# Kernel optimization log

Measured on AMD Instinct MI355X. Metric: run time of the kernel, lower is better.

The kernel has to match this reference:

```python
import jax, jax.numpy as jnp
import numpy as np

D_MODEL = 1024
N_HEADS = 16
D_K = D_MODEL // N_HEADS
ROPE_THETA = 10000.0


def setup_inputs() -> dict:
    key = jax.random.key(0)
    ks = jax.random.split(key, 5)
    B, S = 2, 2048
    std = (2.0 / (D_MODEL + D_MODEL)) ** 0.5
    x = jax.random.normal(ks[0], (B, S, D_MODEL), dtype=jnp.float32)
    Wq = jax.random.normal(ks[1], (D_MODEL, D_MODEL), dtype=jnp.float32) * std
    Wk = jax.random.normal(ks[2], (D_MODEL, D_MODEL), dtype=jnp.float32) * std
    Wv = jax.random.normal(ks[3], (D_MODEL, D_MODEL), dtype=jnp.float32) * std
    Wo = jax.random.normal(ks[4], (D_MODEL, D_MODEL), dtype=jnp.float32) * std
    token_positions = jnp.arange(S, dtype=jnp.int64 if jax.config.jax_enable_x64 else jnp.int32)
    return {"x": x, "Wq": Wq, "Wk": Wk, "Wv": Wv, "Wo": Wo,
            "token_positions": token_positions}


def _apply_rope(t, token_positions):
    # t: [B, H, S, d_k]; token_positions: [S]
    inv_freq = 1.0 / (ROPE_THETA ** (jnp.arange(0, D_K, 2, dtype=jnp.float32) / D_K))  # [d_k/2]
    freqs = token_positions.astype(jnp.float32)[:, None] * inv_freq[None, :]  # [S, d_k/2]
    cos, sin = jnp.cos(freqs), jnp.sin(freqs)
    x1, x2 = t[..., ::2], t[..., 1::2]
    xr = x1 * cos - x2 * sin
    yr = x1 * sin + x2 * cos
    # interleave back to even/odd positions
    out = jnp.stack([xr, yr], axis=-1).reshape(t.shape)
    return out


def reference(x, Wq, Wk, Wv, Wo, token_positions):
    B, S, D = x.shape
    H, dk = N_HEADS, D_K
    # projections: weight is [d_out, d_in], applied as x @ W.T
    def proj_heads(W):
        y = jnp.einsum('bsd,ed->bse', x, W)
        return y.reshape(B, S, H, dk).transpose(0, 2, 1, 3)  # [B,H,S,dk]
    q = proj_heads(Wq)
    k = proj_heads(Wk)
    v = proj_heads(Wv)
    q = _apply_rope(q, token_positions)
    k = _apply_rope(k, token_positions)
    scores = jnp.einsum('bhqd,bhkd->bhqk', q, k) / jnp.sqrt(jnp.float32(dk))
    causal = jnp.tril(jnp.ones((S, S), dtype=bool))
    scores = jnp.where(causal, scores, -jnp.inf)
    attn = jax.nn.softmax(scores, axis=-1)
    out = jnp.einsum('bhqk,bhkd->bhqd', attn, v)  # [B,H,S,dk]
    out = out.transpose(0, 2, 1, 3).reshape(B, S, D)
    return jnp.einsum('bsd,ed->bse', out, Wo)
```

## Files before the change

kernel.cpp:

```cpp
#include <hip/hip_runtime.h>

typedef __bf16 bf16x8 __attribute__((ext_vector_type(8)));
typedef float f32x4 __attribute__((ext_vector_type(4)));
typedef unsigned short u16x8 __attribute__((ext_vector_type(8)));


__device__ __forceinline__ unsigned short f2bf(float f) {
  unsigned u = __builtin_bit_cast(unsigned, f);
  u = (u + 0x7FFFu + ((u >> 16) & 1u)) >> 16;
  return (unsigned short)u;
}

__device__ __forceinline__ unsigned cvt_pk_bf16(float lo, float hi) {
  unsigned r;
  asm("v_cvt_pk_bf16_f32 %0, %1, %2" : "=v"(r) : "v"(lo), "v"(hi));
  return r;
}

__device__ __forceinline__ void load_lds16(const void* g, void* l) {
  __builtin_amdgcn_global_load_lds(
      (__attribute__((address_space(1))) void*)g,
      (__attribute__((address_space(3))) void*)l, 16, 0, 0);
}

__global__ __launch_bounds__(256) void k_convert(
    const float* __restrict__ x,
    const float* __restrict__ wq, const float* __restrict__ wk,
    const float* __restrict__ wv, const float* __restrict__ wo,
    unsigned short* __restrict__ xb,
    unsigned short* __restrict__ wqb, unsigned short* __restrict__ wkb,
    unsigned short* __restrict__ wvb, unsigned short* __restrict__ wob) {
  const int g = blockIdx.x * 256 + threadIdx.x;
  const float* src;
  unsigned short* dst;
  int off;
  if (g < (1 << 20)) {
    src = x; dst = xb; off = g;
  } else {
    const int q = g - (1 << 20);
    const int t = q >> 18;
    off = q & ((1 << 18) - 1);
    src = (t == 0) ? wq : (t == 1) ? wk : (t == 2) ? wv : wo;
    dst = (t == 0) ? wqb : (t == 1) ? wkb : (t == 2) ? wvb : wob;
  }
  const float4 v = ((const float4*)src)[off];
  ushort4 r;
  r.x = f2bf(v.x); r.y = f2bf(v.y); r.z = f2bf(v.z); r.w = f2bf(v.w);
  ((ushort4*)dst)[off] = r;
}

__global__ __launch_bounds__(256) void k_rope_tab(const int* __restrict__ tpos,
                                                  float* __restrict__ ct,
                                                  float* __restrict__ st) {
  const int idx = blockIdx.x * 256 + threadIdx.x;
  const int s = idx >> 5, i = idx & 31;
  const double p = (double)tpos[s];
  const double f = p * pow(10000.0, -(double)(2 * i) / 64.0);
  ct[idx] = (float)cos(f);
  st[idx] = (float)sin(f);
}

__device__ __forceinline__ void gemm_core_1024(
    const unsigned short* __restrict__ Ag,
    const unsigned short* __restrict__ Bg,
    unsigned short* As, unsigned short* Bs, f32x4 (&acc)[4][4], int tid) {
  const int lane = tid & 63;
  const int w = tid >> 6;
  const int wm = (w >> 1) * 64;
  const int wn = (w & 1) * 64;
  const int lr = lane & 15;
  const int lg8 = (lane >> 4) * 8;
  const int c0 = tid, c1 = 256 + tid;
  const int ar0 = c0 >> 2, ac0 = (c0 & 3) * 8;
  const int ar1 = c1 >> 2, ac1 = (c1 & 3) * 8;

  auto stage = [&](int buf, int kt) {
    unsigned short* Ab = As + buf * 4096;
    unsigned short* Bb = Bs + buf * 4096;
    load_lds16(Ag + ar0 * 1024 + kt + ac0, Ab + c0 * 8);
    load_lds16(Ag + ar1 * 1024 + kt + ac1, Ab + c1 * 8);
    load_lds16(Bg + ar0 * 1024 + kt + ac0, Bb + c0 * 8);
    load_lds16(Bg + ar1 * 1024 + kt + ac1, Bb + c1 * 8);
  };

  stage(0, 0);
  stage(1, 32);
  int cur = 0;
  for (int ki = 0; ki < 32; ++ki) {
    if (ki + 2 < 32) {
      int nb = cur + 2; if (nb >= 3) nb -= 3;
      stage(nb, (ki + 2) * 32);
      asm volatile("s_waitcnt vmcnt(8)" ::: "memory");
    } else if (ki + 1 < 32) {
      asm volatile("s_waitcnt vmcnt(4)" ::: "memory");
    } else {
      asm volatile("s_waitcnt vmcnt(0)" ::: "memory");
    }
    __builtin_amdgcn_s_barrier();
    const unsigned short* Ab = As + cur * 4096;
    const unsigned short* Bb = Bs + cur * 4096;
    bf16x8 af[4], bfv[4];
#pragma unroll
    for (int mi = 0; mi < 4; ++mi)
      af[mi] = *(const bf16x8*)(Ab + (wm + mi * 16 + lr) * 32 + lg8);
#pragma unroll
    for (int ni = 0; ni < 4; ++ni)
      bfv[ni] = *(const bf16x8*)(Bb + (wn + ni * 16 + lr) * 32 + lg8);
    __builtin_amdgcn_s_setprio(1);
#pragma unroll
    for (int mi = 0; mi < 4; ++mi)
#pragma unroll
      for (int ni = 0; ni < 4; ++ni)
        acc[mi][ni] = __builtin_amdgcn_mfma_f32_16x16x32_bf16(
            af[mi], bfv[ni], acc[mi][ni], 0, 0, 0);
    __builtin_amdgcn_s_setprio(0);
    __builtin_amdgcn_s_barrier();
    ++cur; if (cur == 3) cur = 0;
  }
}

__global__ __launch_bounds__(256) void k_proj(
    const unsigned short* __restrict__ Xb,
    const unsigned short* __restrict__ Wq, const unsigned short* __restrict__ Wk,
    const unsigned short* __restrict__ Wv,
    const float* __restrict__ ctab, const float* __restrict__ stab,
    unsigned short* __restrict__ Qo, unsigned short* __restrict__ Ko,
    unsigned short* __restrict__ Vo) {
  __shared__ __align__(16) unsigned short As[3 * 128 * 32];
  __shared__ __align__(16) unsigned short Bs[3 * 128 * 32];
  const int z = blockIdx.z;
  const unsigned short* Wsel = (z == 0) ? Wq : (z == 1) ? Wk : Wv;
  unsigned short* Out = (z == 0) ? Qo : (z == 1) ? Ko : Vo;
  const int tid = threadIdx.x;
  const int bm = blockIdx.x * 128, bn = blockIdx.y * 128;
  f32x4 acc[4][4] = {};
  gemm_core_1024(Xb + (size_t)bm * 1024, Wsel + (size_t)bn * 1024, As, Bs, acc, tid);

  const int lane = tid & 63, w = tid >> 6;
  const int wm = (w >> 1) * 64, wn = (w & 1) * 64;
  const int lr = lane & 15, lg = lane >> 4;
  const bool rope = (z < 2);
  const bool odd = lane & 1;
#pragma unroll
  for (int mi = 0; mi < 4; ++mi) {
#pragma unroll
    for (int ni = 0; ni < 4; ++ni) {
#pragma unroll
      for (int reg = 0; reg < 4; ++reg) {
        const int r = bm + wm + mi * 16 + lg * 4 + reg;
        const int e = bn + wn + ni * 16 + lr;
        float val = acc[mi][ni][reg];
        const float partner = __shfl_xor(val, 1);
        const int s = r & 2047, b = r >> 11;
        const int h = e >> 6, d = e & 63;
        float outv = val;
        if (rope) {
          const int i = d >> 1;
          const float c = ctab[s * 32 + i];
          const float sn = stab[s * 32 + i];
          outv = odd ? (val * c + partner * sn) : (val * c - partner * sn);
        }
        if (z == 2)
          Out[((size_t)(b * 16 + h) * 64 + d) * 2048 + s] = f2bf(outv);
        else
          Out[((size_t)(b * 16 + h) * 2048 + s) * 64 + d] = f2bf(outv);
      }
    }
  }
}

__global__ __launch_bounds__(64, 4) void k_attn(
    const unsigned short* __restrict__ Q, const unsigned short* __restrict__ K,
    const unsigned short* __restrict__ Vt, unsigned short* __restrict__ O) {
  __shared__ __align__(16) unsigned short Vs[64 * 64];
  __shared__ __align__(16) unsigned short Pl[16 * 68];
  const int L = blockIdx.x;
  const int bh = (L & 7) * 4 + ((L >> 3) & 3);
  const int p = L >> 5;
  const int qrow = p * 16;
  const int T = (qrow + 79) >> 6;
  const int lane = threadIdx.x & 63;
  const int lr = lane & 15, lg = lane >> 4;
  const unsigned short* Qg = Q + (size_t)bh * 2048 * 64;
  const unsigned short* Kg = K + (size_t)bh * 2048 * 64;
  const unsigned short* Vg = Vt + (size_t)bh * 64 * 2048;

  bf16x8 qf[2];
#pragma unroll
  for (int h = 0; h < 2; ++h)
    qf[h] = *(const bf16x8*)(Qg + (qrow + lr) * 64 + h * 32 + lg * 8);

  u16x8 ouv;
#pragma unroll
  for (int j = 0; j < 8; ++j) ouv[j] = 0x3F80;
  const bf16x8 onesf = __builtin_bit_cast(bf16x8, ouv);

  f32x4 oacc[4] = {};
  float m[4], l[4];
#pragma unroll
  for (int r = 0; r < 4; ++r) { m[r] = -__builtin_inff(); l[r] = 0.f; }

  const float SCL = 0.125f * 1.44269504088896f;

  const int kbase = lr * 64 + lg * 8;
  const unsigned short* Knext = Kg;
  const int vbase = (lane >> 3) * 2048 + (((lane & 7) ^ (lane >> 3)) * 8);
  const unsigned short* Vnext = Vg;
  unsigned short* Vw = &Vs[0];

  auto issueV = [&]() {
#pragma unroll
    for (int i0 = 0; i0 < 8; ++i0)
      load_lds16(Vnext + i0 * 16384 + vbase, Vw + i0 * 512 + lane * 8);
    Vnext += 64;
  };

  issueV();

  for (int t = 0; t < T; ++t) {
    bf16x8 kd[4][2];
#pragma unroll
    for (int nt = 0; nt < 4; ++nt)
#pragma unroll
      for (int h = 0; h < 2; ++h)
        kd[nt][h] = *(const bf16x8*)(Knext + nt * 1024 + h * 32 + kbase);
    Knext += 4096;

    f32x4 sacc[4];
    __builtin_amdgcn_s_setprio(1);
#pragma unroll
    for (int nt = 0; nt < 4; ++nt) {
      f32x4 z = {0.f, 0.f, 0.f, 0.f};
      z = __builtin_amdgcn_mfma_f32_16x16x32_bf16(qf[0], kd[nt][0], z, 0, 0, 0);
      sacc[nt] = __builtin_amdgcn_mfma_f32_16x16x32_bf16(qf[1], kd[nt][1], z, 0, 0, 0);
    }
    __builtin_amdgcn_s_setprio(0);

    const bool needmask = (t == T - 1);
    float pm[4];
#pragma unroll
    for (int r = 0; r < 4; ++r) pm[r] = -__builtin_inff();
#pragma unroll
    for (int nt = 0; nt < 4; ++nt)
#pragma unroll
      for (int reg = 0; reg < 4; ++reg) {
        float sv = sacc[nt][reg];
        if (needmask) {
          const int kg = t * 64 + nt * 16 + lr;
          const int qg = qrow + lg * 4 + reg;
          if (kg > qg) sv = -__builtin_inff();
        }
        sacc[nt][reg] = sv;
        pm[reg] = fmaxf(pm[reg], sv);
      }
#pragma unroll
    for (int off = 1; off < 16; off <<= 1)
#pragma unroll
      for (int reg = 0; reg < 4; ++reg)
        pm[reg] = fmaxf(pm[reg], __shfl_xor(pm[reg], off));

    float gm = -1.f;
#pragma unroll
    for (int reg = 0; reg < 4; ++reg) gm = fmaxf(gm, pm[reg] - m[reg]);
    float msc[4];
    if (__any(gm > 0.f)) {
#pragma unroll
      for (int reg = 0; reg < 4; ++reg) {
        const float mn = fmaxf(m[reg], pm[reg]);
        const float al = exp2f(SCL * (m[reg] - mn));
        m[reg] = mn;
        msc[reg] = SCL * mn;
        l[reg] *= al;
#pragma unroll
        for (int nt = 0; nt < 4; ++nt) oacc[nt][reg] *= al;
      }
    } else {
#pragma unroll
      for (int reg = 0; reg < 4; ++reg) msc[reg] = SCL * m[reg];
    }

#pragma unroll
    for (int nt = 0; nt < 4; ++nt) {
      const float p0 = exp2f(sacc[nt][0] * SCL - msc[0]);
      const float p1 = exp2f(sacc[nt][1] * SCL - msc[1]);
      const float p2 = exp2f(sacc[nt][2] * SCL - msc[2]);
      const float p3 = exp2f(sacc[nt][3] * SCL - msc[3]);
      const unsigned w01 = cvt_pk_bf16(p0, p1);
      const unsigned w23 = cvt_pk_bf16(p2, p3);
      unsigned short* base = Pl + (lg * 4) * 68 + nt * 16 + lr;
      base[0] = (unsigned short)w01;
      base[68] = (unsigned short)(w01 >> 16);
      base[136] = (unsigned short)w23;
      base[204] = (unsigned short)(w23 >> 16);
    }
    bf16x8 pa[2];
#pragma unroll
    for (int ks = 0; ks < 2; ++ks)
      pa[ks] = *(const bf16x8*)(Pl + lr * 68 + ks * 32 + lg * 8);

    asm volatile("s_waitcnt vmcnt(0)" ::: "memory");

    __builtin_amdgcn_s_setprio(1);
    {
      f32x4 z = {0.f, 0.f, 0.f, 0.f};
      z = __builtin_amdgcn_mfma_f32_16x16x32_bf16(pa[0], onesf, z, 0, 0, 0);
      z = __builtin_amdgcn_mfma_f32_16x16x32_bf16(pa[1], onesf, z, 0, 0, 0);
#pragma unroll
      for (int reg = 0; reg < 4; ++reg) l[reg] += z[reg];
    }
#pragma unroll
    for (int nt = 0; nt < 4; ++nt) {
      const int row = nt * 16 + lr;
      const bf16x8 vb0 = *(const bf16x8*)(Vw + row * 64 + ((lg ^ (row & 7)) * 8));
      const bf16x8 vb1 = *(const bf16x8*)(Vw + row * 64 + (((lg + 4) ^ (row & 7)) * 8));
      oacc[nt] = __builtin_amdgcn_mfma_f32_16x16x32_bf16(pa[0], vb0, oacc[nt], 0, 0, 0);
      oacc[nt] = __builtin_amdgcn_mfma_f32_16x16x32_bf16(pa[1], vb1, oacc[nt], 0, 0, 0);
    }
    __builtin_amdgcn_s_setprio(0);

    asm volatile("s_waitcnt lgkmcnt(0)" ::: "memory");
    if (t + 1 < T) issueV();
  }

  const int b = bh >> 4, h = bh & 15;
#pragma unroll
  for (int reg = 0; reg < 4; ++reg) {
    const float inv = 1.0f / l[reg];
    const int s = qrow + lg * 4 + reg;
#pragma unroll
    for (int nt = 0; nt < 4; ++nt) {
      const int dv = nt * 16 + lr;
      O[((size_t)b * 2048 + s) * 1024 + h * 64 + dv] = f2bf(oacc[nt][reg] * inv);
    }
  }
}

__global__ __launch_bounds__(256) void k_out(const unsigned short* __restrict__ Ab,
                                             const unsigned short* __restrict__ Wo,
                                             float* __restrict__ Out) {
  __shared__ __align__(16) unsigned short As[3 * 128 * 32];
  __shared__ __align__(16) unsigned short Bs[3 * 128 * 32];
  const int tid = threadIdx.x;
  const int bm = blockIdx.x * 128, bn = blockIdx.y * 128;
  f32x4 acc[4][4] = {};
  gemm_core_1024(Ab + (size_t)bm * 1024, Wo + (size_t)bn * 1024, As, Bs, acc, tid);
  const int lane = tid & 63, w = tid >> 6;
  const int wm = (w >> 1) * 64, wn = (w & 1) * 64;
  const int lr = lane & 15, lg = lane >> 4;
#pragma unroll
  for (int mi = 0; mi < 4; ++mi)
#pragma unroll
    for (int ni = 0; ni < 4; ++ni)
#pragma unroll
      for (int reg = 0; reg < 4; ++reg) {
        const int r = bm + wm + mi * 16 + lg * 4 + reg;
        const int e = bn + wn + ni * 16 + lr;
        Out[(size_t)r * 1024 + e] = acc[mi][ni][reg];
      }
}

extern "C" void kernel_launch(void* const* d_in, const int* in_sizes, int n_in,
                              void* d_out, int out_size, void* d_ws, size_t ws_size,
                              hipStream_t stream) {
  const float* x = (const float*)d_in[0];
  const float* Wq = (const float*)d_in[1];
  const float* Wk = (const float*)d_in[2];
  const float* Wv = (const float*)d_in[3];
  const float* Wo = (const float*)d_in[4];
  const int* tpos = (const int*)d_in[5];
  float* out = (float*)d_out;
  char* ws = (char*)d_ws;
  const size_t MB = 1024 * 1024;
  unsigned short* xb = (unsigned short*)(ws);
  unsigned short* wqb = (unsigned short*)(ws + 8 * MB);
  unsigned short* wkb = (unsigned short*)(ws + 10 * MB);
  unsigned short* wvb = (unsigned short*)(ws + 12 * MB);
  unsigned short* wob = (unsigned short*)(ws + 14 * MB);
  unsigned short* Qb = (unsigned short*)(ws + 16 * MB);
  unsigned short* Kb = (unsigned short*)(ws + 24 * MB);
  unsigned short* Vtb = (unsigned short*)(ws + 32 * MB);
  unsigned short* Ab = (unsigned short*)(ws + 40 * MB);
  float* ctab = (float*)(ws + 48 * MB);
  float* stab = (float*)(ws + 48 * MB + 256 * 1024);

  k_convert<<<dim3(8192), dim3(256), 0, stream>>>(x, Wq, Wk, Wv, Wo, xb, wqb, wkb,
                                                  wvb, wob);
  k_rope_tab<<<dim3(256), dim3(256), 0, stream>>>(tpos, ctab, stab);
  k_proj<<<dim3(32, 8, 3), dim3(256), 0, stream>>>(xb, wqb, wkb, wvb, ctab, stab,
                                                   Qb, Kb, Vtb);
  k_attn<<<dim3(4096), dim3(64), 0, stream>>>(Qb, Kb, Vtb, Ab);
  k_out<<<dim3(32, 8), dim3(256), 0, stream>>>(Ab, wob, out);
}
```

Baseline: 179.8 us.

## Pair causal query tiles per attention block and double-buffer K/V loads

Each attention block now handles two 16-row query tiles, one short and its mirror long (p and 127-p), so every block does a similar amount of causal work. The grid is halved accordingly. K fragments are prefetched into alternating register sets and V into a double-buffered LDS area, with a partial vmcnt wait, so the next tile's loads overlap the current tile's compute. Separately, the V projection epilogue now writes packed 4-element vectors along the transposed layout instead of scalar stores. The cost is higher register pressure (launch bounds lowered to 2 waves), twice the LDS for V, and fewer, longer blocks.

```diff
diff --git a/kernel.cpp b/kernel.cpp
--- a/kernel.cpp
+++ b/kernel.cpp
@@ -139,7 +139,27 @@
   const int lane = tid & 63, w = tid >> 6;
   const int wm = (w >> 1) * 64, wn = (w & 1) * 64;
   const int lr = lane & 15, lg = lane >> 4;
-  const bool rope = (z < 2);
+
+  if (z == 2) {
+#pragma unroll
+    for (int mi = 0; mi < 4; ++mi) {
+      const int r0 = bm + wm + mi * 16 + lg * 4;
+      const int s = r0 & 2047, b = r0 >> 11;
+#pragma unroll
+      for (int ni = 0; ni < 4; ++ni) {
+        const int e = bn + wn + ni * 16 + lr;
+        const int h = e >> 6, d = e & 63;
+        ushort4 pk;
+        pk.x = f2bf(acc[mi][ni][0]);
+        pk.y = f2bf(acc[mi][ni][1]);
+        pk.z = f2bf(acc[mi][ni][2]);
+        pk.w = f2bf(acc[mi][ni][3]);
+        *(ushort4*)&Out[((size_t)(b * 16 + h) * 64 + d) * 2048 + s] = pk;
+      }
+    }
+    return;
+  }
+
   const bool odd = lane & 1;
 #pragma unroll
   for (int mi = 0; mi < 4; ++mi) {
@@ -153,90 +173,91 @@
         const float partner = __shfl_xor(val, 1);
         const int s = r & 2047, b = r >> 11;
         const int h = e >> 6, d = e & 63;
-        float outv = val;
-        if (rope) {
-          const int i = d >> 1;
-          const float c = ctab[s * 32 + i];
-          const float sn = stab[s * 32 + i];
-          outv = odd ? (val * c + partner * sn) : (val * c - partner * sn);
-        }
-        if (z == 2)
-          Out[((size_t)(b * 16 + h) * 64 + d) * 2048 + s] = f2bf(outv);
-        else
-          Out[((size_t)(b * 16 + h) * 2048 + s) * 64 + d] = f2bf(outv);
+        const int i = d >> 1;
+        const float c = ctab[s * 32 + i];
+        const float sn = stab[s * 32 + i];
+        const float outv = odd ? (val * c + partner * sn) : (val * c - partner * sn);
+        Out[((size_t)(b * 16 + h) * 2048 + s) * 64 + d] = f2bf(outv);
       }
     }
   }
 }
 
-__global__ __launch_bounds__(64, 4) void k_attn(
+__global__ __launch_bounds__(64, 2) void k_attn(
     const unsigned short* __restrict__ Q, const unsigned short* __restrict__ K,
     const unsigned short* __restrict__ Vt, unsigned short* __restrict__ O) {
-  __shared__ __align__(16) unsigned short Vs[64 * 64];
+  __shared__ __align__(16) unsigned short Vs[2][64 * 64];
   __shared__ __align__(16) unsigned short Pl[16 * 68];
   const int L = blockIdx.x;
   const int bh = (L & 7) * 4 + ((L >> 3) & 3);
   const int p = L >> 5;
-  const int qrow = p * 16;
-  const int T = (qrow + 79) >> 6;
+  const int qrowA = p * 16, qrowB = (127 - p) * 16;
+  const int Ta = (qrowA + 79) >> 6;
+  const int Tb = (qrowB + 79) >> 6;
+  const int TT = Ta + Tb;
   const int lane = threadIdx.x & 63;
   const int lr = lane & 15, lg = lane >> 4;
   const unsigned short* Qg = Q + (size_t)bh * 2048 * 64;
   const unsigned short* Kg = K + (size_t)bh * 2048 * 64;
   const unsigned short* Vg = Vt + (size_t)bh * 64 * 2048;
 
-  bf16x8 qf[2];
-#pragma unroll
-  for (int h = 0; h < 2; ++h)
-    qf[h] = *(const bf16x8*)(Qg + (qrow + lr) * 64 + h * 32 + lg * 8);
+  bf16x8 qfA[2], qfB[2];
+#pragma unroll
+  for (int h = 0; h < 2; ++h) {
+    qfA[h] = *(const bf16x8*)(Qg + (qrowA + lr) * 64 + h * 32 + lg * 8);
+    qfB[h] = *(const bf16x8*)(Qg + (qrowB + lr) * 64 + h * 32 + lg * 8);
+  }
 
   u16x8 ouv;
 #pragma unroll
   for (int j = 0; j < 8; ++j) ouv[j] = 0x3F80;
   const bf16x8 onesf = __builtin_bit_cast(bf16x8, ouv);
 
-  f32x4 oacc[4] = {};
-  float m[4], l[4];
-#pragma unroll
-  for (int r = 0; r < 4; ++r) { m[r] = -__builtin_inff(); l[r] = 0.f; }
+  f32x4 oA[4] = {}, oB[4] = {};
+  float mA[4], lA[4], mB[4], lB[4];
+#pragma unroll
+  for (int r = 0; r < 4; ++r) {
+    mA[r] = -__builtin_inff(); lA[r] = 0.f;
+    mB[r] = -__builtin_inff(); lB[r] = 0.f;
+  }
 
   const float SCL = 0.125f * 1.44269504088896f;
 
   const int kbase = lr * 64 + lg * 8;
-  const unsigned short* Knext = Kg;
   const int vbase = (lane >> 3) * 2048 + (((lane & 7) ^ (lane >> 3)) * 8);
-  const unsigned short* Vnext = Vg;
-  unsigned short* Vw = &Vs[0];
-
-  auto issueV = [&]() {
+
+  auto kvof = [&](int t) { return (t < Tb) ? t : t - Tb; };
+  auto loadK = [&](bf16x8 (&kd)[4][2], int kv) {
+    const unsigned short* base = Kg + (size_t)kv * 4096 + kbase;
+#pragma unroll
+    for (int nt = 0; nt < 4; ++nt)
+#pragma unroll
+      for (int h = 0; h < 2; ++h)
+        kd[nt][h] = *(const bf16x8*)(base + nt * 1024 + h * 32);
+  };
+  auto issueV = [&](int buf, int kv) {
+    const unsigned short* src = Vg + kv * 64 + vbase;
+    unsigned short* dst = &Vs[buf][0] + lane * 8;
 #pragma unroll
     for (int i0 = 0; i0 < 8; ++i0)
-      load_lds16(Vnext + i0 * 16384 + vbase, Vw + i0 * 512 + lane * 8);
-    Vnext += 64;
+      load_lds16(src + i0 * 16384, dst + i0 * 512);
   };
 
-  issueV();
-
-  for (int t = 0; t < T; ++t) {
-    bf16x8 kd[4][2];
-#pragma unroll
-    for (int nt = 0; nt < 4; ++nt)
-#pragma unroll
-      for (int h = 0; h < 2; ++h)
-        kd[nt][h] = *(const bf16x8*)(Knext + nt * 1024 + h * 32 + kbase);
-    Knext += 4096;
-
+  auto core = [&](bf16x8 (&kc)[4][2], int kv, int T, bf16x8 (&qf)[2],
+                  float (&m)[4], float (&l)[4], f32x4 (&oacc)[4], int qrow,
+                  int vbuf, bool more) {
+    const int kv0 = kv * 64;
     f32x4 sacc[4];
     __builtin_amdgcn_s_setprio(1);
 #pragma unroll
     for (int nt = 0; nt < 4; ++nt) {
       f32x4 z = {0.f, 0.f, 0.f, 0.f};
-      z = __builtin_amdgcn_mfma_f32_16x16x32_bf16(qf[0], kd[nt][0], z, 0, 0, 0);
-      sacc[nt] = __builtin_amdgcn_mfma_f32_16x16x32_bf16(qf[1], kd[nt][1], z, 0, 0, 0);
+      z = __builtin_amdgcn_mfma_f32_16x16x32_bf16(qf[0], kc[nt][0], z, 0, 0, 0);
+      sacc[nt] = __builtin_amdgcn_mfma_f32_16x16x32_bf16(qf[1], kc[nt][1], z, 0, 0, 0);
     }
     __builtin_amdgcn_s_setprio(0);
 
-    const bool needmask = (t == T - 1);
+    const bool needmask = (kv == T - 1);
     float pm[4];
 #pragma unroll
     for (int r = 0; r < 4; ++r) pm[r] = -__builtin_inff();
@@ -246,7 +267,7 @@
       for (int reg = 0; reg < 4; ++reg) {
         float sv = sacc[nt][reg];
         if (needmask) {
-          const int kg = t * 64 + nt * 16 + lr;
+          const int kg = kv0 + nt * 16 + lr;
           const int qg = qrow + lg * 4 + reg;
           if (kg > qg) sv = -__builtin_inff();
         }
@@ -298,8 +319,10 @@
     for (int ks = 0; ks < 2; ++ks)
       pa[ks] = *(const bf16x8*)(Pl + lr * 68 + ks * 32 + lg * 8);
 
-    asm volatile("s_waitcnt vmcnt(0)" ::: "memory");
-
+    if (more) asm volatile("s_waitcnt vmcnt(16)" ::: "memory");
+    else      asm volatile("s_waitcnt vmcnt(0)" ::: "memory");
+
+    const unsigned short* Vw = &Vs[vbuf][0];
     __builtin_amdgcn_s_setprio(1);
     {
       f32x4 z = {0.f, 0.f, 0.f, 0.f};
@@ -317,20 +340,42 @@
       oacc[nt] = __builtin_amdgcn_mfma_f32_16x16x32_bf16(pa[1], vb1, oacc[nt], 0, 0, 0);
     }
     __builtin_amdgcn_s_setprio(0);
-
-    asm volatile("s_waitcnt lgkmcnt(0)" ::: "memory");
-    if (t + 1 < T) issueV();
+  };
+
+  bf16x8 kbufA[4][2], kbufB[4][2];
+  loadK(kbufA, 0);
+  issueV(0, 0);
+
+  auto iter = [&](int t, bf16x8 (&kc)[4][2], bf16x8 (&kn)[4][2]) {
+    const int nxt = t + 1;
+    const bool more = (nxt < TT);
+    if (more) {
+      const int kvn = kvof(nxt);
+      loadK(kn, kvn);
+      issueV(nxt & 1, kvn);
+    }
+    if (t < Tb) core(kc, t, Tb, qfB, mB, lB, oB, qrowB, t & 1, more);
+    else        core(kc, t - Tb, Ta, qfA, mA, lA, oA, qrowA, t & 1, more);
+  };
+
+  int t = 0;
+  for (;;) {
+    iter(t, kbufA, kbufB); ++t; if (t >= TT) break;
+    iter(t, kbufB, kbufA); ++t; if (t >= TT) break;
   }
 
   const int b = bh >> 4, h = bh & 15;
 #pragma unroll
   for (int reg = 0; reg < 4; ++reg) {
-    const float inv = 1.0f / l[reg];
-    const int s = qrow + lg * 4 + reg;
+    const float invA = 1.0f / lA[reg];
+    const float invB = 1.0f / lB[reg];
+    const int sA = qrowA + lg * 4 + reg;
+    const int sB = qrowB + lg * 4 + reg;
 #pragma unroll
     for (int nt = 0; nt < 4; ++nt) {
       const int dv = nt * 16 + lr;
-      O[((size_t)b * 2048 + s) * 1024 + h * 64 + dv] = f2bf(oacc[nt][reg] * inv);
+      O[((size_t)b * 2048 + sA) * 1024 + h * 64 + dv] = f2bf(oA[nt][reg] * invA);
+      O[((size_t)b * 2048 + sB) * 1024 + h * 64 + dv] = f2bf(oB[nt][reg] * invB);
     }
   }
 }
@@ -388,6 +433,6 @@
   k_rope_tab<<<dim3(256), dim3(256), 0, stream>>>(tpos, ctab, stab);
   k_proj<<<dim3(32, 8, 3), dim3(256), 0, stream>>>(xb, wqb, wkb, wvb, ctab, stab,
                                                    Qb, Kb, Vtb);
-  k_attn<<<dim3(4096), dim3(64), 0, stream>>>(Qb, Kb, Vtb, Ab);
+  k_attn<<<dim3(2048), dim3(64), 0, stream>>>(Qb, Kb, Vtb, Ab);
   k_out<<<dim3(32, 8), dim3(256), 0, stream>>>(Ab, wob, out);
 }
```

Result: faster. 175.2 us (-2.6%).
